# Optimization experiments

Hardware: AMD Instinct MI355X
Metric: run time of the kernel (lower is better)

Reference implementation:

```python
import jax, jax.numpy as jnp
import numpy as np
import math

D_MODEL, D_STATE, D_CONV = 1024, 16, 4
D_INNER = 2 * D_MODEL
DT_RANK = math.ceil(D_MODEL / 16)
B, L = 4, 2048


def setup_inputs() -> dict:
    key = jax.random.key(0)
    ks = jax.random.split(key, 10)
    s = 0.02
    x = jax.random.normal(ks[0], (B, L, D_MODEL), dtype=jnp.float32)
    ln_g = jnp.ones((D_MODEL,), jnp.float32)
    ln_b = jnp.zeros((D_MODEL,), jnp.float32)
    W_in = jax.random.normal(ks[1], (D_MODEL, 2 * D_INNER), jnp.float32) * s
    conv_w = jax.random.normal(ks[2], (D_INNER, 1, D_CONV), jnp.float32) * s
    conv_b = jnp.zeros((D_INNER,), jnp.float32)
    W_xp = jax.random.normal(ks[3], (D_INNER, DT_RANK + 2 * D_STATE), jnp.float32) * s
    W_dt = jax.random.normal(ks[4], (DT_RANK, D_INNER), jnp.float32) * (DT_RANK ** -0.5)
    # inverse-softplus of dt ~ 0.01 (between dt_min=0.001 and dt_max=0.1)
    dt_bias = jnp.full((D_INNER,), float(np.log(np.expm1(0.01))), jnp.float32)
    # S4D-real init: A = 1..d_state per channel
    A_log = jnp.log(jnp.broadcast_to(jnp.arange(1, D_STATE + 1, dtype=jnp.float32), (D_INNER, D_STATE)))
    D_skip = jnp.ones((D_INNER,), jnp.float32)
    W_out = jax.random.normal(ks[5], (D_INNER, D_MODEL), jnp.float32) * s
    return dict(x=x, ln_g=ln_g, ln_b=ln_b, W_in=W_in, conv_w=conv_w, conv_b=conv_b,
                W_xp=W_xp, W_dt=W_dt, dt_bias=dt_bias, A_log=A_log, D_skip=D_skip, W_out=W_out)


def _layernorm(x, g, b, eps=1e-5):
    m = jnp.mean(x, axis=-1, keepdims=True)
    v = jnp.mean(jnp.square(x - m), axis=-1, keepdims=True)
    return (x - m) * jax.lax.rsqrt(v + eps) * g + b


def _mamba(xn, W_in, conv_w, conv_b, W_xp, W_dt, dt_bias, A_log, D_skip, W_out):
    # xn: [B, L, d_model]
    xz = xn @ W_in                                   # [B, L, 2*d_inner]
    xi, z = jnp.split(xz, 2, axis=-1)                # each [B, L, d_inner]
    # depthwise causal conv over sequence
    xi_t = jnp.transpose(xi, (0, 2, 1))              # [B, d_inner, L]
    xc = jax.lax.conv_general_dilated(
        xi_t, conv_w, window_strides=(1,), padding=[(D_CONV - 1, 0)],
        feature_group_count=D_INNER, dimension_numbers=('NCH', 'OIH', 'NCH'))
    xc = jnp.transpose(xc, (0, 2, 1)) + conv_b       # [B, L, d_inner]
    xc = jax.nn.silu(xc)
    # input-dependent dt, B, C
    x_dbl = xc @ W_xp                                # [B, L, dt_rank + 2*d_state]
    dt_lo, Bm, Cm = jnp.split(x_dbl, [DT_RANK, DT_RANK + D_STATE], axis=-1)
    delta = jax.nn.softplus(dt_lo @ W_dt + dt_bias)  # [B, L, d_inner]
    A = -jnp.exp(A_log)                              # [d_inner, d_state]

    def step(h, inp):
        dt_t, B_t, C_t, u_t = inp                    # [B,D], [B,N], [B,N], [B,D]
        dA = jnp.exp(dt_t[..., None] * A)            # [B, D, N]
        h = h * dA + (dt_t * u_t)[..., None] * B_t[:, None, :]
        y = jnp.einsum('bdn,bn->bd', h, C_t)
        return h, y

    h0 = jnp.zeros((xn.shape[0], D_INNER, D_STATE), xn.dtype)
    inputs = (jnp.transpose(delta, (1, 0, 2)), jnp.transpose(Bm, (1, 0, 2)),
              jnp.transpose(Cm, (1, 0, 2)), jnp.transpose(xc, (1, 0, 2)))
    _, ys = jax.lax.scan(step, h0, inputs)           # ys: [L, B, d_inner]
    y = jnp.transpose(ys, (1, 0, 2)) + xc * D_skip   # [B, L, d_inner]
    y = y * jax.nn.silu(z)
    return y @ W_out                                 # [B, L, d_model]


def reference(x, ln_g, ln_b, W_in, conv_w, conv_b, W_xp, W_dt, dt_bias, A_log, D_skip, W_out):
    xn = _layernorm(x, ln_g, ln_b)
    return _mamba(xn, W_in, conv_w, conv_b, W_xp, W_dt, dt_bias, A_log, D_skip, W_out) + x
```

## Files before the change

### kernel.cpp

```cpp
#include <hip/hip_runtime.h>

#define DM 1024
#define DI 2048
#define DS 16
#define DTR 64
#define LL 2048
#define NROW 8192

typedef unsigned short u16;
typedef unsigned int u32;
typedef __bf16 bf16x8 __attribute__((ext_vector_type(8)));
typedef float f32x4 __attribute__((ext_vector_type(4)));
typedef float v2f __attribute__((ext_vector_type(2)));

__device__ __forceinline__ float bf2f(u16 u) {
  unsigned int v = ((unsigned int)u) << 16;
  return __builtin_bit_cast(float, v);
}
__device__ __forceinline__ u16 f2bf(float f) {
  unsigned int x = __builtin_bit_cast(unsigned int, f);
  x = x + 0x7fffu + ((x >> 16) & 1u);
  return (u16)(x >> 16);
}
__device__ __forceinline__ float lo_bf(u32 v) { return __builtin_bit_cast(float, v << 16); }
__device__ __forceinline__ float hi_bf(u32 v) { return __builtin_bit_cast(float, v & 0xFFFF0000u); }
__device__ __forceinline__ u32 pack_bf(float a, float b) {
  return (u32)f2bf(a) | ((u32)f2bf(b) << 16);
}
__device__ __forceinline__ bool io_f32(const u16* lng) { return lng[0] == 0; }

__device__ __forceinline__ void async16(const void* g, void* l) {
  __builtin_amdgcn_global_load_lds(
      (const __attribute__((address_space(1))) unsigned int*)g,
      (__attribute__((address_space(3))) unsigned int*)l, 16, 0, 0);
}

__device__ __forceinline__ void pow16v(float e1, v2f* E) {
  float e2 = e1 * e1;
  v2f sq = {e2, e2};
  E[0] = (v2f){e1, e2};
#pragma unroll
  for (int k = 1; k < 8; k++) E[k] = E[k - 1] * sq;
}

__device__ void transpose_dev(const void* __restrict__ in, u16* __restrict__ out,
                              int R, int C, int Cp, int bx, int by, bool f32,
                              int tid, u16 (*tile)[33]) {
  int c0 = bx * 32, r0 = by * 32;
  int tx = tid & 31, ty = tid >> 5;
#pragma unroll
  for (int i = 0; i < 4; i++) {
    int r = r0 + ty + i * 8, c = c0 + tx;
    u16 v = 0;
    if (r < R && c < C) {
      if (f32) v = f2bf(((const float*)in)[(size_t)r * C + c]);
      else     v = ((const u16*)in)[(size_t)r * C + c];
    }
    tile[ty + i * 8][tx] = v;
  }
  __syncthreads();
#pragma unroll
  for (int i = 0; i < 4; i++) {
    int oc = c0 + ty + i * 8, orr = r0 + tx;
    if (oc < Cp && orr < R) out[(size_t)oc * R + orr] = tile[tx][ty + i * 8];
  }
}

__global__ __launch_bounds__(256) void prep_k(
    const void* __restrict__ W_in, u16* __restrict__ W_inT,
    const void* __restrict__ W_dt, u16* __restrict__ W_dtT,
    const void* __restrict__ W_xp, u16* __restrict__ W_xpT,
    const void* __restrict__ W_out, u16* __restrict__ W_outT,
    const void* __restrict__ x, const u16* __restrict__ g,
    const u16* __restrict__ b, u16* __restrict__ xn) {
  __shared__ u16 tile[32][33];
  __shared__ float rs_[4], rq_[4];
  bool f32 = io_f32(g);
  int tid = threadIdx.x;
  int bid = blockIdx.x;
  if (bid < 4096) {
    transpose_dev(W_in, W_inT, 1024, 4096, 4096, bid & 127, bid >> 7, f32, tid, tile);
    return;
  } else if (bid < 4224) {
    bid -= 4096;
    transpose_dev(W_dt, W_dtT, 64, 2048, 2048, bid & 63, bid >> 6, f32, tid, tile);
    return;
  } else if (bid < 4480) {
    bid -= 4224;
    transpose_dev(W_xp, W_xpT, 2048, 96, 128, bid & 3, bid >> 2, f32, tid, tile);
    return;
  } else if (bid < 6528) {
    bid -= 4480;
    transpose_dev(W_out, W_outT, 2048, 1024, 1024, bid & 31, bid >> 5, f32, tid, tile);
    return;
  }
  int row = bid - 6528;
  float f[4];
  if (f32) {
    float4 v = ((const float4*)((const float*)x + (size_t)row * DM))[tid];
    f[0] = v.x; f[1] = v.y; f[2] = v.z; f[3] = v.w;
  } else {
    ushort4 v = ((const ushort4*)((const u16*)x + (size_t)row * DM))[tid];
    f[0] = bf2f(v.x); f[1] = bf2f(v.y); f[2] = bf2f(v.z); f[3] = bf2f(v.w);
  }
  float s = f[0] + f[1] + f[2] + f[3];
  float q = f[0] * f[0] + f[1] * f[1] + f[2] * f[2] + f[3] * f[3];
#pragma unroll
  for (int off = 32; off; off >>= 1) {
    s += __shfl_down(s, off, 64);
    q += __shfl_down(q, off, 64);
  }
  int wid = tid >> 6, lane = tid & 63;
  if (lane == 0) { rs_[wid] = s; rq_[wid] = q; }
  __syncthreads();
  float ts = rs_[0] + rs_[1] + rs_[2] + rs_[3];
  float tq = rq_[0] + rq_[1] + rq_[2] + rq_[3];
  float mean = ts * (1.f / DM);
  float var = tq * (1.f / DM) - mean * mean;
  float inv = rsqrtf(var + 1e-5f);
  int c = tid * 4;
  ushort4 o;
  u16* po = (u16*)&o;
#pragma unroll
  for (int k = 0; k < 4; k++) {
    float gk = f32 ? ((const float*)g)[c + k] : bf2f(g[c + k]);
    float bk = f32 ? ((const float*)b)[c + k] : bf2f(b[c + k]);
    po[k] = f2bf((f[k] - mean) * inv * gk + bk);
  }
  ((ushort4*)(xn + (size_t)row * DM))[tid] = o;
}

template <int EPI>
__device__ __forceinline__ void gemm_body(const u16* __restrict__ A,
                                          const u16* __restrict__ BT,
                                          void* __restrict__ C,
                                          const void* __restrict__ extra,
                                          int M, int N, int Klen, int ldk,
                                          const u16* __restrict__ lng, int mOff,
                                          u16* ldsA, u16* ldsB) {
  int tid = threadIdx.x;
  int wid = tid >> 6, lane = tid & 63;
  int l15 = lane & 15, quad = lane >> 4;
  int bm = blockIdx.x * 128;
  int bn;
  const u16* Ae = A;
  const u16* Be = BT;
  float* Cpart = nullptr;
  if (EPI == 5) {
    bn = 0;
    int ky = blockIdx.y;
    Ae += (size_t)ky * Klen;
    Be += (size_t)ky * Klen;
    Cpart = (float*)C + (size_t)ky * M * N;
  } else {
    bn = blockIdx.y * 128;
  }
  int wrow = (wid >> 1) * 64, wcol = (wid & 1) * 64;

  f32x4 zero = {0.f, 0.f, 0.f, 0.f};
  f32x4 acc[4][4];
#pragma unroll
  for (int i = 0; i < 4; i++)
#pragma unroll
    for (int j = 0; j < 4; j++) acc[i][j] = zero;

  int row0 = tid >> 2;
  int colb = (tid & 3) * 16;
  const char* Ap0 = (const char*)Ae + ((size_t)(bm + row0) * ldk) * 2 + colb;
  const char* Ap1 = (const char*)Ae + ((size_t)(bm + row0 + 64) * ldk) * 2 + colb;
  const char* Bp0 = (const char*)Be + ((size_t)(bn + row0) * ldk) * 2 + colb;
  const char* Bp1 = (const char*)Be + ((size_t)(bn + row0 + 64) * ldk) * 2 + colb;
  u16* la = ldsA + wid * 512;
  u16* lb = ldsB + wid * 512;

  for (int k0 = 0; k0 < Klen; k0 += 64) {
    size_t kb = (size_t)k0 * 2;
    async16(Ap0 + kb, la);
    async16(Ap1 + kb, la + 2048);
    async16(Ap0 + kb + 64, la + 4096);
    async16(Ap1 + kb + 64, la + 6144);
    async16(Bp0 + kb, lb);
    async16(Bp1 + kb, lb + 2048);
    async16(Bp0 + kb + 64, lb + 4096);
    async16(Bp1 + kb + 64, lb + 6144);
    __syncthreads();
#pragma unroll
    for (int s = 0; s < 2; s++) {
      bf16x8 af[4], bfr[4];
#pragma unroll
      for (int i = 0; i < 4; i++)
        af[i] = *(const bf16x8*)&ldsA[s * 4096 + (wrow + i * 16 + l15) * 32 + quad * 8];
#pragma unroll
      for (int j = 0; j < 4; j++)
        bfr[j] = *(const bf16x8*)&ldsB[s * 4096 + (wcol + j * 16 + l15) * 32 + quad * 8];
#pragma unroll
      for (int i = 0; i < 4; i++)
#pragma unroll
        for (int j = 0; j < 4; j++)
          acc[i][j] = __builtin_amdgcn_mfma_f32_16x16x32_bf16(af[i], bfr[j], acc[i][j], 0, 0, 0);
    }
    __syncthreads();
  }

  bool f32 = (EPI == 2 || EPI == 3) ? io_f32(lng) : false;
#pragma unroll
  for (int i = 0; i < 4; i++) {
#pragma unroll
    for (int j = 0; j < 4; j++) {
      int gn = bn + wcol + j * 16 + l15;
#pragma unroll
      for (int r = 0; r < 4; r++) {
        int gm = bm + wrow + i * 16 + quad * 4 + r;
        float v = acc[i][j][r];
        if (EPI == 2) {
          float bias = f32 ? ((const float*)extra)[gn] : bf2f(((const u16*)extra)[gn]);
          v += bias;
          float sp = (v > 20.f) ? v : log1pf(__expf(v));
          ((u16*)C)[(size_t)gm * N + gn] = f2bf(sp);
        } else if (EPI == 3) {
          size_t idx = (size_t)(gm + mOff) * N + gn;
          v += f32 ? ((const float*)extra)[idx] : bf2f(((const u16*)extra)[idx]);
          if (f32) ((float*)C)[idx] = v;
          else     ((u16*)C)[idx] = f2bf(v);
        } else {
          Cpart[(size_t)gm * N + gn] = v;
        }
      }
    }
  }
}

#define GEMM_WRAP(name, EPI)                                                        \
  __global__ __launch_bounds__(256) void name(                                      \
      const u16* __restrict__ A, const u16* __restrict__ BT, void* __restrict__ C,  \
      const void* __restrict__ extra, int M, int N, int Klen, int ldk,              \
      const u16* __restrict__ lng, int mOff) {                                      \
    __shared__ __align__(16) u16 ldsA[128 * 64];                                    \
    __shared__ __align__(16) u16 ldsB[128 * 64];                                    \
    gemm_body<EPI>(A, BT, C, extra, M, N, Klen, ldk, lng, mOff, ldsA, ldsB);        \
  }

GEMM_WRAP(gemm_xp_k, 5)
GEMM_WRAP(gemm_dt_k, 2)
GEMM_WRAP(gemm_out_k, 3)

__global__ __launch_bounds__(512, 2) void gemm_in256_k(
    const u16* __restrict__ A, const u16* __restrict__ BT,
    u16* __restrict__ C, u16* __restrict__ Z, int ldk, int Klen) {
  __shared__ __align__(16) u16 lds[65536];
  const int tid = threadIdx.x;
  const int wid = tid >> 6, lane = tid & 63;
  const int l15 = lane & 15, quad = lane >> 4;
  const int bm = blockIdx.x * 256, bn = blockIdx.y * 256;
  const int wrow = (wid >> 2) * 128;
  const int wcol = (wid & 3) * 64;

  const int srow = tid >> 3;
  const int sg = ((tid & 7) ^ (srow & 7)) * 8;
  const u16* Ag[4];
  const u16* Bg[4];
#pragma unroll
  for (int s = 0; s < 4; s++) {
    Ag[s] = A + (size_t)(bm + s * 64 + srow) * ldk + sg;
    Bg[s] = BT + (size_t)(bn + s * 64 + srow) * ldk + sg;
  }
  const int sdst = wid * 512;

  int rA[2], rB[2];
#pragma unroll
  for (int ks = 0; ks < 2; ks++) {
    int gsw = ((ks * 4 + quad) ^ (l15 & 7)) * 8;
    rA[ks] = (wrow + l15) * 64 + gsw;
    rB[ks] = 16384 + (wcol + l15) * 64 + gsw;
  }

  f32x4 acc[8][4];
  f32x4 zero = {0.f, 0.f, 0.f, 0.f};
#pragma unroll
  for (int i = 0; i < 8; i++)
#pragma unroll
    for (int j = 0; j < 4; j++) acc[i][j] = zero;

  const int NT = Klen >> 6;
  async16(Ag[0], &lds[sdst]);
  async16(Ag[1], &lds[4096 + sdst]);
  async16(Bg[0], &lds[16384 + sdst]);
  async16(Bg[1], &lds[16384 + 4096 + sdst]);
  async16(Bg[2], &lds[16384 + 8192 + sdst]);
  async16(Bg[3], &lds[16384 + 12288 + sdst]);
  async16(Ag[2], &lds[8192 + sdst]);
  async16(Ag[3], &lds[12288 + sdst]);
  if (NT > 1) {
    async16(Ag[0] + 64, &lds[32768 + sdst]);
    async16(Ag[1] + 64, &lds[32768 + 4096 + sdst]);
  }

  bf16x8 a[4][2], b0[2][2], b1[2][2];
  for (int t = 0; t < NT; ++t) {
    const int bb = (t & 1) << 15;
    const int nb = bb ^ 32768;
    const int k1 = (t + 1) << 6;
    const int k2 = (t + 2) << 6;
    const bool st1 = (t + 1 < NT), st2 = (t + 2 < NT);
    if (st1) asm volatile("s_waitcnt vmcnt(2)" ::: "memory");
    else     asm volatile("s_waitcnt vmcnt(0)" ::: "memory");
    __builtin_amdgcn_s_barrier();

#pragma unroll
    for (int mf = 0; mf < 4; mf++) {
      a[mf][0] = *(const bf16x8*)&lds[bb + rA[0] + mf * 1024];
      a[mf][1] = *(const bf16x8*)&lds[bb + rA[1] + mf * 1024];
    }
#pragma unroll
    for (int nf = 0; nf < 2; nf++) {
      b0[nf][0] = *(const bf16x8*)&lds[bb + rB[0] + nf * 1024];
      b0[nf][1] = *(const bf16x8*)&lds[bb + rB[1] + nf * 1024];
    }
    if (st1) {
      async16(Bg[0] + k1, &lds[nb + 16384 + sdst]);
      async16(Bg[1] + k1, &lds[nb + 16384 + 4096 + sdst]);
    }
    __builtin_amdgcn_s_barrier();
    asm volatile("s_waitcnt lgkmcnt(0)" ::: "memory");
    __builtin_amdgcn_s_setprio(1);
#pragma unroll
    for (int ks = 0; ks < 2; ks++)
#pragma unroll
      for (int mf = 0; mf < 4; mf++)
#pragma unroll
        for (int nf = 0; nf < 2; nf++)
          acc[mf][nf] = __builtin_amdgcn_mfma_f32_16x16x32_bf16(a[mf][ks], b0[nf][ks], acc[mf][nf], 0, 0, 0);
    __builtin_amdgcn_s_setprio(0);
    __builtin_amdgcn_s_barrier();

#pragma unroll
    for (int nf = 0; nf < 2; nf++) {
      b1[nf][0] = *(const bf16x8*)&lds[bb + rB[0] + (2 + nf) * 1024];
      b1[nf][1] = *(const bf16x8*)&lds[bb + rB[1] + (2 + nf) * 1024];
    }
    if (st1) {
      async16(Bg[2] + k1, &lds[nb + 16384 + 8192 + sdst]);
      async16(Bg[3] + k1, &lds[nb + 16384 + 12288 + sdst]);
    }
    __builtin_amdgcn_s_barrier();
    asm volatile("s_waitcnt lgkmcnt(0)" ::: "memory");
    __builtin_amdgcn_s_setprio(1);
#pragma unroll
    for (int ks = 0; ks < 2; ks++)
#pragma unroll
      for (int mf = 0; mf < 4; mf++)
#pragma unroll
        for (int nf = 0; nf < 2; nf++)
          acc[mf][2 + nf] = __builtin_amdgcn_mfma_f32_16x16x32_bf16(a[mf][ks], b1[nf][ks], acc[mf][2 + nf], 0, 0, 0);
    __builtin_amdgcn_s_setprio(0);
    __builtin_amdgcn_s_barrier();

#pragma unroll
    for (int mf = 0; mf < 4; mf++) {
      a[mf][0] = *(const bf16x8*)&lds[bb + rA[0] + 4096 + mf * 1024];
      a[mf][1] = *(const bf16x8*)&lds[bb + rA[1] + 4096 + mf * 1024];
    }
    if (st1) {
      async16(Ag[2] + k1, &lds[nb + 8192 + sdst]);
      async16(Ag[3] + k1, &lds[nb + 12288 + sdst]);
    }
    __builtin_amdgcn_s_barrier();
    asm volatile("s_waitcnt lgkmcnt(0)" ::: "memory");
    __builtin_amdgcn_s_setprio(1);
#pragma unroll
    for (int ks = 0; ks < 2; ks++)
#pragma unroll
      for (int mf = 0; mf < 4; mf++)
#pragma unroll
        for (int nf = 0; nf < 2; nf++)
          acc[4 + mf][2 + nf] = __builtin_amdgcn_mfma_f32_16x16x32_bf16(a[mf][ks], b1[nf][ks], acc[4 + mf][2 + nf], 0, 0, 0);
    __builtin_amdgcn_s_setprio(0);
    __builtin_amdgcn_s_barrier();

    if (st2) {
      async16(Ag[0] + k2, &lds[bb + sdst]);
      async16(Ag[1] + k2, &lds[bb + 4096 + sdst]);
    }
    __builtin_amdgcn_s_setprio(1);
#pragma unroll
    for (int ks = 0; ks < 2; ks++)
#pragma unroll
      for (int mf = 0; mf < 4; mf++)
#pragma unroll
        for (int nf = 0; nf < 2; nf++)
          acc[4 + mf][nf] = __builtin_amdgcn_mfma_f32_16x16x32_bf16(a[mf][ks], b0[nf][ks], acc[4 + mf][nf], 0, 0, 0);
    __builtin_amdgcn_s_setprio(0);
  }

#pragma unroll
  for (int i = 0; i < 8; i++) {
#pragma unroll
    for (int j = 0; j < 4; j++) {
      int gn = bn + wcol + j * 16 + l15;
#pragma unroll
      for (int r = 0; r < 4; r++) {
        int gm = bm + wrow + i * 16 + quad * 4 + r;
        float v = acc[i][j][r];
        if (gn < DI) {
          C[(size_t)gm * DI + gn] = f2bf(v);
        } else {
          float sv = v / (1.f + __expf(-v));
          Z[(size_t)gm * DI + (gn - DI)] = f2bf(sv);
        }
      }
    }
  }
}

__global__ __launch_bounds__(256) void conv4_k(const u16* __restrict__ xi,
                                               const void* __restrict__ cw,
                                               const void* __restrict__ cb,
                                               u16* __restrict__ xc,
                                               const u16* __restrict__ lng) {
  bool f32 = io_f32(lng);
  int idx = blockIdx.x * 256 + threadIdx.x;
  int c = idx & (DI - 1);
  int rq = idx >> 11;
  int l4 = (rq & (LL / 4 - 1)) * 4;
  int b = rq >> 9;
  float w[4], bias;
  if (f32) {
    float4 w4 = *(const float4*)((const float*)cw + (size_t)c * 4);
    w[0] = w4.x; w[1] = w4.y; w[2] = w4.z; w[3] = w4.w;
    bias = ((const float*)cb)[c];
  } else {
    ushort4 w4 = *(const ushort4*)((const u16*)cw + (size_t)c * 4);
    w[0] = bf2f(w4.x); w[1] = bf2f(w4.y); w[2] = bf2f(w4.z); w[3] = bf2f(w4.w);
    bias = bf2f(((const u16*)cb)[c]);
  }
  size_t base = ((size_t)(b * LL + l4)) * DI + c;
  float v[7];
#pragma unroll
  for (int j = 0; j < 7; j++) {
    int lj = l4 - 3 + j;
    v[j] = (lj >= 0) ? bf2f(xi[base + (size_t)(j - 3) * DI]) : 0.f;
  }
#pragma unroll
  for (int r = 0; r < 4; r++) {
    float acc = bias + v[r] * w[0] + v[r + 1] * w[1] + v[r + 2] * w[2] + v[r + 3] * w[3];
    float sv = acc / (1.f + __expf(-acc));
    xc[base + (size_t)r * DI] = f2bf(sv);
  }
}

__global__ __launch_bounds__(256) void reduce_dtlo_k(const float* __restrict__ Cpart,
                                                     float* __restrict__ xdbl,
                                                     u16* __restrict__ dtlo, int M) {
  int i = blockIdx.x * 256 + threadIdx.x;
  size_t MN = (size_t)M * 128;
  float v = Cpart[i] + Cpart[MN + i] + Cpart[2 * MN + i] + Cpart[3 * MN + i];
  xdbl[i] = v;
  int j = i & 127, m = i >> 7;
  if (j < 64) dtlo[(size_t)m * 64 + j] = f2bf(v);
}

__device__ __forceinline__ bool fastA(const void* A_log, bool f32, int d0) {
  bool fast = true;
#pragma unroll
  for (int c = 0; c < 2; c++)
    for (int n = 0; n < 16; n++) {
      float al = f32 ? ((const float*)A_log)[(d0 + c) * DS + n]
                     : bf2f(((const u16*)A_log)[(d0 + c) * DS + n]);
      float Av = __expf(al);
      fast = fast && (__builtin_fabsf(Av - (float)(n + 1)) <= 1e-3f * (n + 1));
    }
  return fast;
}

template <int S>
__global__ __launch_bounds__(256) void scan_p1(const u16* __restrict__ delta,
                                               const u16* __restrict__ xc,
                                               const float* __restrict__ xdbl,
                                               const void* __restrict__ A_log,
                                               const u16* __restrict__ lng,
                                               float* __restrict__ Pbuf,
                                               float* __restrict__ Lbuf,
                                               int NS) {
  bool f32 = io_f32(lng);
  int tid = threadIdx.x;
  int seg = blockIdx.x, dch = blockIdx.y, bL = blockIdx.z;
  int d0 = (dch * 256 + tid) * 2;
  size_t rb = (size_t)bL * LL;
  int l0 = seg * S;
  extern __shared__ float bc[];
#pragma unroll 2
  for (int i = tid; i < S * 4; i += 256) {
    int t = i >> 2, k = (i & 3) * 4;
    *(float4*)&bc[t * 16 + k] = *(const float4*)&xdbl[(rb + l0 + t) * 128 + 64 + k];
  }
  __syncthreads();
  size_t sb = ((((size_t)bL * NS + seg) * DI) + d0) * DS;
  const u32* dpu = (const u32*)(delta + (rb + l0) * DI + d0);
  const u32* upu = (const u32*)(xc + (rb + l0) * DI + d0);
  if (fastA(A_log, f32, d0)) {
    v2f h0[8], h1[8];
#pragma unroll
    for (int k = 0; k < 8; k++) { h0[k] = (v2f){0.f, 0.f}; h1[k] = (v2f){0.f, 0.f}; }
    float sum0 = 0.f, sum1 = 0.f;
    const int T = 8;
    for (int t0 = 0; t0 < S; t0 += T) {
      u32 dv[T], uv[T];
#pragma unroll
      for (int j = 0; j < T; j++) {
        dv[j] = dpu[j * (DI / 2)];
        uv[j] = upu[j * (DI / 2)];
      }
      dpu += T * (DI / 2);
      upu += T * (DI / 2);
#pragma unroll
      for (int j = 0; j < T; j++) {
        float dt0 = lo_bf(dv[j]), dt1 = hi_bf(dv[j]);
        float u0 = lo_bf(uv[j]), u1 = hi_bf(uv[j]);
        sum0 += dt0; sum1 += dt1;
        const v2f* B2 = (const v2f*)&bc[(t0 + j) * 16];
        v2f E[8];
        pow16v(__expf(-dt0), E);
        float com0 = dt0 * u0;
        v2f cv0 = {com0, com0};
#pragma unroll
        for (int k = 0; k < 8; k++) h0[k] = h0[k] * E[k] + B2[k] * cv0;
        pow16v(__expf(-dt1), E);
        float com1 = dt1 * u1;
        v2f cv1 = {com1, com1};
#pragma unroll
        for (int k = 0; k < 8; k++) h1[k] = h1[k] * E[k] + B2[k] * cv1;
      }
    }
    v2f P[8];
    pow16v(__expf(-sum0), P);
#pragma unroll
    for (int k = 0; k < 8; k++) { *(v2f*)&Pbuf[sb + 2 * k] = P[k]; *(v2f*)&Lbuf[sb + 2 * k] = h0[k]; }
    pow16v(__expf(-sum1), P);
#pragma unroll
    for (int k = 0; k < 8; k++) { *(v2f*)&Pbuf[sb + 16 + 2 * k] = P[k]; *(v2f*)&Lbuf[sb + 16 + 2 * k] = h1[k]; }
  } else {
    for (int c = 0; c < 2; c++) {
      int d = d0 + c;
      float A2[16], h[16], P[16];
#pragma unroll
      for (int n = 0; n < 16; n++) {
        float al = f32 ? ((const float*)A_log)[d * DS + n] : bf2f(((const u16*)A_log)[d * DS + n]);
        A2[n] = -__expf(al);
        h[n] = 0.f; P[n] = 1.f;
      }
      const u16* dp = delta + (rb + l0) * DI + d;
      const u16* up = xc + (rb + l0) * DI + d;
      for (int t = 0; t < S; t++) {
        float dt = bf2f(dp[(size_t)t * DI]);
        float u = bf2f(up[(size_t)t * DI]);
        float com = dt * u;
        const float* Bf = &bc[t * 16];
#pragma unroll
        for (int n = 0; n < 16; n++) {
          float dA = __expf(dt * A2[n]);
          h[n] = fmaf(h[n], dA, com * Bf[n]);
          P[n] *= dA;
        }
      }
#pragma unroll
      for (int n = 0; n < 16; n++) { Pbuf[sb + 16 * c + n] = P[n]; Lbuf[sb + 16 * c + n] = h[n]; }
    }
  }
}

__global__ __launch_bounds__(256) void scan_p2(float* __restrict__ Pbuf,
                                               float* __restrict__ Lbuf, int NS) {
  int idx = blockIdx.x * 256 + threadIdx.x;
  int bL = idx >> 15;
  int dn = idx & 32767;
  float H = 0.f;
  for (int s = 0; s < NS; s++) {
    size_t o = ((size_t)(bL * NS + s) << 15) + dn;
    float P = Pbuf[o], Lv = Lbuf[o];
    Lbuf[o] = H;
    H = fmaf(P, H, Lv);
  }
}

template <int S>
__global__ __launch_bounds__(256) void scan_p3(u16* __restrict__ dy,
                                               const u16* __restrict__ xc,
                                               const float* __restrict__ xdbl,
                                               const u16* __restrict__ z,
                                               const void* __restrict__ A_log,
                                               const void* __restrict__ D_skip,
                                               const u16* __restrict__ lng,
                                               const float* __restrict__ Lbuf,
                                               int NS) {
  bool f32 = io_f32(lng);
  int tid = threadIdx.x;
  int seg = blockIdx.x, dch = blockIdx.y, bL = blockIdx.z;
  int d0 = (dch * 256 + tid) * 2;
  size_t rb = (size_t)bL * LL;
  int l0 = seg * S;
  extern __shared__ float bc[];
#pragma unroll 2
  for (int i = tid; i < S * 8; i += 256) {
    int t = i >> 3, k = (i & 7) * 4;
    *(float4*)&bc[t * 32 + k] = *(const float4*)&xdbl[(rb + l0 + t) * 128 + 64 + k];
  }
  __syncthreads();
  size_t sb = ((((size_t)bL * NS + seg) * DI) + d0) * DS;
  float Dv0 = f32 ? ((const float*)D_skip)[d0] : bf2f(((const u16*)D_skip)[d0]);
  float Dv1 = f32 ? ((const float*)D_skip)[d0 + 1] : bf2f(((const u16*)D_skip)[d0 + 1]);
  u32* dpu = (u32*)(dy + (rb + l0) * DI + d0);
  const u32* upu = (const u32*)(xc + (rb + l0) * DI + d0);
  const u32* zpu = (const u32*)(z + (rb + l0) * DI + d0);
  if (fastA(A_log, f32, d0)) {
    v2f h0[8], h1[8];
#pragma unroll
    for (int k = 0; k < 8; k++) {
      h0[k] = *(const v2f*)&Lbuf[sb + 2 * k];
      h1[k] = *(const v2f*)&Lbuf[sb + 16 + 2 * k];
    }
    const int T = 8;
    for (int t0 = 0; t0 < S; t0 += T) {
      u32 dv[T], uv[T], zv[T];
#pragma unroll
      for (int j = 0; j < T; j++) {
        dv[j] = dpu[j * (DI / 2)];
        uv[j] = upu[j * (DI / 2)];
        zv[j] = zpu[j * (DI / 2)];
      }
      upu += T * (DI / 2);
      zpu += T * (DI / 2);
#pragma unroll
      for (int j = 0; j < T; j++) {
        float dt0 = lo_bf(dv[j]), dt1 = hi_bf(dv[j]);
        float u0 = lo_bf(uv[j]), u1 = hi_bf(uv[j]);
        float zg0 = lo_bf(zv[j]), zg1 = hi_bf(zv[j]);
        const v2f* B2 = (const v2f*)&bc[(t0 + j) * 32];
        const v2f* C2 = (const v2f*)&bc[(t0 + j) * 32 + 16];
        v2f E[8];
        pow16v(__expf(-dt0), E);
        float com0 = dt0 * u0;
        v2f cv = {com0, com0};
        v2f a0 = {0.f, 0.f}, a1 = {0.f, 0.f};
#pragma unroll
        for (int k = 0; k < 8; k += 2) {
          h0[k] = h0[k] * E[k] + B2[k] * cv;
          h0[k + 1] = h0[k + 1] * E[k + 1] + B2[k + 1] * cv;
          a0 += h0[k] * C2[k];
          a1 += h0[k + 1] * C2[k + 1];
        }
        float cs0 = (a0.x + a0.y) + (a1.x + a1.y);
        pow16v(__expf(-dt1), E);
        float com1 = dt1 * u1;
        cv = (v2f){com1, com1};
        a0 = (v2f){0.f, 0.f}; a1 = (v2f){0.f, 0.f};
#pragma unroll
        for (int k = 0; k < 8; k += 2) {
          h1[k] = h1[k] * E[k] + B2[k] * cv;
          h1[k + 1] = h1[k + 1] * E[k + 1] + B2[k + 1] * cv;
          a0 += h1[k] * C2[k];
          a1 += h1[k + 1] * C2[k + 1];
        }
        float cs1 = (a0.x + a0.y) + (a1.x + a1.y);
        float y0 = (cs0 + u0 * Dv0) * zg0;
        float y1 = (cs1 + u1 * Dv1) * zg1;
        dpu[j * (DI / 2)] = pack_bf(y0, y1);
      }
      dpu += T * (DI / 2);
    }
  } else {
    for (int c = 0; c < 2; c++) {
      int d = d0 + c;
      float A2[16], h[16];
#pragma unroll
      for (int n = 0; n < 16; n++) {
        float al = f32 ? ((const float*)A_log)[d * DS + n] : bf2f(((const u16*)A_log)[d * DS + n]);
        A2[n] = -__expf(al);
        h[n] = Lbuf[sb + 16 * c + n];
      }
      float Dv = (c == 0) ? Dv0 : Dv1;
      u16* dp = dy + (rb + l0) * DI + d;
      const u16* up = xc + (rb + l0) * DI + d;
      const u16* zp = z + (rb + l0) * DI + d;
      for (int t = 0; t < S; t++) {
        float dt = bf2f(dp[(size_t)t * DI]);
        float u = bf2f(up[(size_t)t * DI]);
        float zg = bf2f(zp[(size_t)t * DI]);
        float com = dt * u;
        const float* Bf = &bc[t * 32];
        const float* Cf = &bc[t * 32 + 16];
        float cs = 0.f;
#pragma unroll
        for (int n = 0; n < 16; n++) {
          float dA = __expf(dt * A2[n]);
          h[n] = fmaf(h[n], dA, com * Bf[n]);
          cs = fmaf(h[n], Cf[n], cs);
        }
        dp[(size_t)t * DI] = f2bf((cs + u * Dv) * zg);
      }
    }
  }
}

static void launch_scan(int NS, int nb, u16* xi, u16* xc, float* xdbl, u16* z,
                        const u16* A_log, const u16* D_sk, const u16* ln_g,
                        float* Pbuf, float* Lbuf, hipStream_t stream) {
  int S = LL / NS;
  dim3 g1(NS, 4, nb);
  if (S == 32) {
    scan_p1<32><<<g1, 256, 32 * 64, stream>>>(xi, xc, xdbl, A_log, ln_g, Pbuf, Lbuf, NS);
  } else if (S == 64) {
    scan_p1<64><<<g1, 256, 64 * 64, stream>>>(xi, xc, xdbl, A_log, ln_g, Pbuf, Lbuf, NS);
  } else {
    scan_p1<128><<<g1, 256, 128 * 64, stream>>>(xi, xc, xdbl, A_log, ln_g, Pbuf, Lbuf, NS);
  }
  scan_p2<<<nb * 128, 256, 0, stream>>>(Pbuf, Lbuf, NS);
  if (S == 32) {
    scan_p3<32><<<g1, 256, 32 * 128, stream>>>(xi, xc, xdbl, z, A_log, D_sk, ln_g, Lbuf, NS);
  } else if (S == 64) {
    scan_p3<64><<<g1, 256, 64 * 128, stream>>>(xi, xc, xdbl, z, A_log, D_sk, ln_g, Lbuf, NS);
  } else {
    scan_p3<128><<<g1, 256, 128 * 128, stream>>>(xi, xc, xdbl, z, A_log, D_sk, ln_g, Lbuf, NS);
  }
}

extern "C" void kernel_launch(void* const* d_in, const int* in_sizes, int n_in,
                              void* d_out, int out_size, void* d_ws, size_t ws_size,
                              hipStream_t stream) {
  const u16* x = (const u16*)d_in[0];
  const u16* ln_g = (const u16*)d_in[1];
  const u16* ln_b = (const u16*)d_in[2];
  const u16* W_in = (const u16*)d_in[3];
  const u16* cw = (const u16*)d_in[4];
  const u16* cb = (const u16*)d_in[5];
  const u16* W_xp = (const u16*)d_in[6];
  const u16* W_dt = (const u16*)d_in[7];
  const u16* dt_b = (const u16*)d_in[8];
  const u16* A_log = (const u16*)d_in[9];
  const u16* D_sk = (const u16*)d_in[10];
  const u16* W_out = (const u16*)d_in[11];

  char* ws = (char*)d_ws;
  const size_t MB = 1024 * 1024;

  if (ws_size >= 124 * MB) {
    int NS = (ws_size >= 180 * MB) ? 64 : (ws_size >= 144 * MB) ? 32 : 16;
    u16* xc = (u16*)(ws + 0);
    u16* xn = xc;
    u16* W_inT = (u16*)(ws + 16 * MB);
    u16* xi = (u16*)(ws + 32 * MB);
    u16* z = (u16*)(ws + 64 * MB);
    float* xdbl = (float*)(ws + 96 * MB);
    u16* dtlo = (u16*)(ws + 100 * MB);
    u16* W_xpT = (u16*)(ws + 101 * MB);
    u16* W_dtT = (u16*)(ws + 102 * MB);
    u16* W_outT = (u16*)(ws + 103 * MB);
    size_t stateSz = (size_t)NS * 4 * DI * DS * 4;
    float* Cpart = (float*)(ws + 107 * MB);
    float* Pbuf = (float*)(ws + 107 * MB);
    float* Lbuf = (float*)(ws + 107 * MB + stateSz);

    prep_k<<<6528 + NROW, 256, 0, stream>>>(W_in, W_inT, W_dt, W_dtT, W_xp, W_xpT,
                                            W_out, W_outT, x, ln_g, ln_b, xn);
    gemm_in256_k<<<dim3(NROW / 256, (2 * DI) / 256), 512, 0, stream>>>(xn, W_inT, xi, z, DM, DM);
    conv4_k<<<(NROW / 4 * DI) / 256, 256, 0, stream>>>(xi, cw, cb, xc, ln_g);
    gemm_xp_k<<<dim3(64, 4), 256, 0, stream>>>(xc, W_xpT, Cpart, nullptr, NROW, 128, 512, DI, ln_g, 0);
    reduce_dtlo_k<<<(NROW * 128) / 256, 256, 0, stream>>>(Cpart, xdbl, dtlo, NROW);
    gemm_dt_k<<<dim3(64, 16), 256, 0, stream>>>(dtlo, W_dtT, xi, dt_b, NROW, DI, DTR, DTR, ln_g, 0);
    launch_scan(NS, 4, xi, xc, xdbl, z, A_log, D_sk, ln_g, Pbuf, Lbuf, stream);
    gemm_out_k<<<dim3(64, 8), 256, 0, stream>>>(xi, W_outT, d_out, x, NROW, DM, DI, DI, ln_g, 0);
  } else {
    int NS = 32;
    u16* W_inT = (u16*)(ws + 0);
    u16* W_xpT = (u16*)(ws + 8 * MB);
    u16* W_dtT = (u16*)(ws + 9 * MB);
    u16* W_outT = (u16*)(ws + 10 * MB);
    u16* xn = (u16*)(ws + 14 * MB);
    u16* xi = (u16*)(ws + 30 * MB);
    u16* z = (u16*)(ws + 38 * MB);
    u16* xc = (u16*)(ws + 46 * MB);
    float* xdbl = (float*)(ws + 54 * MB);
    u16* dtlo = (u16*)(ws + 55 * MB);
    float* Cpart = (float*)(ws + 56 * MB);
    float* Pbuf = (float*)(ws + 56 * MB);
    float* Lbuf = (float*)(ws + 61 * MB);

    prep_k<<<6528 + NROW, 256, 0, stream>>>(W_in, W_inT, W_dt, W_dtT, W_xp, W_xpT,
                                            W_out, W_outT, x, ln_g, ln_b, xn);
    for (int b = 0; b < 4; b++) {
      const u16* xnb = xn + (size_t)b * LL * DM;
      gemm_in256_k<<<dim3(LL / 256, (2 * DI) / 256), 512, 0, stream>>>(xnb, W_inT, xi, z, DM, DM);
      conv4_k<<<(LL / 4 * DI) / 256, 256, 0, stream>>>(xi, cw, cb, xc, ln_g);
      gemm_xp_k<<<dim3(16, 4), 256, 0, stream>>>(xc, W_xpT, Cpart, nullptr, LL, 128, 512, DI, ln_g, 0);
      reduce_dtlo_k<<<(LL * 128) / 256, 256, 0, stream>>>(Cpart, xdbl, dtlo, LL);
      gemm_dt_k<<<dim3(16, 16), 256, 0, stream>>>(dtlo, W_dtT, xi, dt_b, LL, DI, DTR, DTR, ln_g, 0);
      launch_scan(NS, 1, xi, xc, xdbl, z, A_log, D_sk, ln_g, Pbuf, Lbuf, stream);
      gemm_out_k<<<dim3(16, 8), 256, 0, stream>>>(xi, W_outT, d_out, x, LL, DM, DI, DI, ln_g, b * LL);
    }
  }
}
```

Measured before the change: 523.6 us.

## Restructure GEMM main loop with register-prefetched fragments and one barrier per tile

Rewrites the in-projection GEMM K-loop so each tile is loaded as a whole stage, A and B together, two stages ahead. LDS fragments for the next tile are read into registers while MFMAs for the current tile are still running. The four barriers per iteration become one barrier plus a full vmcnt(0) wait. This aims to cut barrier stalls and hide LDS read latency, at the cost of more live registers (aLo/aHi split) and a coarser global-load wait that may expose memory latency.

```diff
diff --git a/kernel.cpp b/kernel.cpp
--- a/kernel.cpp
+++ b/kernel.cpp
@@ -284,102 +284,92 @@
   const int NT = Klen >> 6;
   async16(Ag[0], &lds[sdst]);
   async16(Ag[1], &lds[4096 + sdst]);
-  async16(Bg[0], &lds[16384 + sdst]);
-  async16(Bg[1], &lds[16384 + 4096 + sdst]);
-  async16(Bg[2], &lds[16384 + 8192 + sdst]);
-  async16(Bg[3], &lds[16384 + 12288 + sdst]);
   async16(Ag[2], &lds[8192 + sdst]);
   async16(Ag[3], &lds[12288 + sdst]);
+  async16(Bg[0], &lds[16384 + sdst]);
+  async16(Bg[1], &lds[20480 + sdst]);
+  async16(Bg[2], &lds[24576 + sdst]);
+  async16(Bg[3], &lds[28672 + sdst]);
   if (NT > 1) {
     async16(Ag[0] + 64, &lds[32768 + sdst]);
-    async16(Ag[1] + 64, &lds[32768 + 4096 + sdst]);
-  }
-
-  bf16x8 a[4][2], b0[2][2], b1[2][2];
+    async16(Ag[1] + 64, &lds[36864 + sdst]);
+    async16(Ag[2] + 64, &lds[40960 + sdst]);
+    async16(Ag[3] + 64, &lds[45056 + sdst]);
+    async16(Bg[0] + 64, &lds[49152 + sdst]);
+    async16(Bg[1] + 64, &lds[53248 + sdst]);
+    async16(Bg[2] + 64, &lds[57344 + sdst]);
+    async16(Bg[3] + 64, &lds[61440 + sdst]);
+  }
+  asm volatile("s_waitcnt vmcnt(8)" ::: "memory");
+  __builtin_amdgcn_s_barrier();
+  __builtin_amdgcn_sched_barrier(0);
+
+  bf16x8 aLo[4][2], aHi[4][2], b0[2][2], b1[2][2];
+#pragma unroll
+  for (int mf = 0; mf < 4; mf++) {
+    aLo[mf][0] = *(const bf16x8*)&lds[rA[0] + mf * 1024];
+    aLo[mf][1] = *(const bf16x8*)&lds[rA[1] + mf * 1024];
+  }
+#pragma unroll
+  for (int nf = 0; nf < 2; nf++)
+#pragma unroll
+    for (int ks = 0; ks < 2; ks++) {
+      b0[nf][ks] = *(const bf16x8*)&lds[rB[ks] + nf * 1024];
+      b1[nf][ks] = *(const bf16x8*)&lds[rB[ks] + (2 + nf) * 1024];
+    }
+
   for (int t = 0; t < NT; ++t) {
     const int bb = (t & 1) << 15;
     const int nb = bb ^ 32768;
-    const int k1 = (t + 1) << 6;
     const int k2 = (t + 2) << 6;
     const bool st1 = (t + 1 < NT), st2 = (t + 2 < NT);
-    if (st1) asm volatile("s_waitcnt vmcnt(2)" ::: "memory");
-    else     asm volatile("s_waitcnt vmcnt(0)" ::: "memory");
+
+    __builtin_amdgcn_s_setprio(1);
+#pragma unroll
+    for (int ks = 0; ks < 2; ks++)
+#pragma unroll
+      for (int mf = 0; mf < 4; mf++)
+#pragma unroll
+        for (int nf = 0; nf < 2; nf++)
+          acc[mf][nf] = __builtin_amdgcn_mfma_f32_16x16x32_bf16(aLo[mf][ks], b0[nf][ks], acc[mf][nf], 0, 0, 0);
+    __builtin_amdgcn_s_setprio(0);
+#pragma unroll
+    for (int mf = 0; mf < 4; mf++) {
+      aHi[mf][0] = *(const bf16x8*)&lds[bb + rA[0] + 4096 + mf * 1024];
+      aHi[mf][1] = *(const bf16x8*)&lds[bb + rA[1] + 4096 + mf * 1024];
+    }
+    __builtin_amdgcn_s_setprio(1);
+#pragma unroll
+    for (int ks = 0; ks < 2; ks++)
+#pragma unroll
+      for (int mf = 0; mf < 4; mf++)
+#pragma unroll
+        for (int nf = 0; nf < 2; nf++)
+          acc[mf][2 + nf] = __builtin_amdgcn_mfma_f32_16x16x32_bf16(aLo[mf][ks], b1[nf][ks], acc[mf][2 + nf], 0, 0, 0);
+    __builtin_amdgcn_s_setprio(0);
+
+    asm volatile("s_waitcnt lgkmcnt(0)" ::: "memory");
+    __builtin_amdgcn_sched_barrier(0);
+    asm volatile("s_waitcnt vmcnt(0)" ::: "memory");
     __builtin_amdgcn_s_barrier();
-
-#pragma unroll
-    for (int mf = 0; mf < 4; mf++) {
-      a[mf][0] = *(const bf16x8*)&lds[bb + rA[0] + mf * 1024];
-      a[mf][1] = *(const bf16x8*)&lds[bb + rA[1] + mf * 1024];
-    }
-#pragma unroll
-    for (int nf = 0; nf < 2; nf++) {
-      b0[nf][0] = *(const bf16x8*)&lds[bb + rB[0] + nf * 1024];
-      b0[nf][1] = *(const bf16x8*)&lds[bb + rB[1] + nf * 1024];
-    }
-    if (st1) {
-      async16(Bg[0] + k1, &lds[nb + 16384 + sdst]);
-      async16(Bg[1] + k1, &lds[nb + 16384 + 4096 + sdst]);
-    }
-    __builtin_amdgcn_s_barrier();
-    asm volatile("s_waitcnt lgkmcnt(0)" ::: "memory");
-    __builtin_amdgcn_s_setprio(1);
-#pragma unroll
-    for (int ks = 0; ks < 2; ks++)
-#pragma unroll
-      for (int mf = 0; mf < 4; mf++)
-#pragma unroll
-        for (int nf = 0; nf < 2; nf++)
-          acc[mf][nf] = __builtin_amdgcn_mfma_f32_16x16x32_bf16(a[mf][ks], b0[nf][ks], acc[mf][nf], 0, 0, 0);
-    __builtin_amdgcn_s_setprio(0);
-    __builtin_amdgcn_s_barrier();
-
-#pragma unroll
-    for (int nf = 0; nf < 2; nf++) {
-      b1[nf][0] = *(const bf16x8*)&lds[bb + rB[0] + (2 + nf) * 1024];
-      b1[nf][1] = *(const bf16x8*)&lds[bb + rB[1] + (2 + nf) * 1024];
-    }
-    if (st1) {
-      async16(Bg[2] + k1, &lds[nb + 16384 + 8192 + sdst]);
-      async16(Bg[3] + k1, &lds[nb + 16384 + 12288 + sdst]);
-    }
-    __builtin_amdgcn_s_barrier();
-    asm volatile("s_waitcnt lgkmcnt(0)" ::: "memory");
-    __builtin_amdgcn_s_setprio(1);
-#pragma unroll
-    for (int ks = 0; ks < 2; ks++)
-#pragma unroll
-      for (int mf = 0; mf < 4; mf++)
-#pragma unroll
-        for (int nf = 0; nf < 2; nf++)
-          acc[mf][2 + nf] = __builtin_amdgcn_mfma_f32_16x16x32_bf16(a[mf][ks], b1[nf][ks], acc[mf][2 + nf], 0, 0, 0);
-    __builtin_amdgcn_s_setprio(0);
-    __builtin_amdgcn_s_barrier();
-
-#pragma unroll
-    for (int mf = 0; mf < 4; mf++) {
-      a[mf][0] = *(const bf16x8*)&lds[bb + rA[0] + 4096 + mf * 1024];
-      a[mf][1] = *(const bf16x8*)&lds[bb + rA[1] + 4096 + mf * 1024];
-    }
-    if (st1) {
-      async16(Ag[2] + k1, &lds[nb + 8192 + sdst]);
-      async16(Ag[3] + k1, &lds[nb + 12288 + sdst]);
-    }
-    __builtin_amdgcn_s_barrier();
-    asm volatile("s_waitcnt lgkmcnt(0)" ::: "memory");
-    __builtin_amdgcn_s_setprio(1);
-#pragma unroll
-    for (int ks = 0; ks < 2; ks++)
-#pragma unroll
-      for (int mf = 0; mf < 4; mf++)
-#pragma unroll
-        for (int nf = 0; nf < 2; nf++)
-          acc[4 + mf][2 + nf] = __builtin_amdgcn_mfma_f32_16x16x32_bf16(a[mf][ks], b1[nf][ks], acc[4 + mf][2 + nf], 0, 0, 0);
-    __builtin_amdgcn_s_setprio(0);
-    __builtin_amdgcn_s_barrier();
+    __builtin_amdgcn_sched_barrier(0);
 
     if (st2) {
       async16(Ag[0] + k2, &lds[bb + sdst]);
       async16(Ag[1] + k2, &lds[bb + 4096 + sdst]);
+      async16(Ag[2] + k2, &lds[bb + 8192 + sdst]);
+      async16(Ag[3] + k2, &lds[bb + 12288 + sdst]);
+      async16(Bg[0] + k2, &lds[bb + 16384 + sdst]);
+      async16(Bg[1] + k2, &lds[bb + 20480 + sdst]);
+      async16(Bg[2] + k2, &lds[bb + 24576 + sdst]);
+      async16(Bg[3] + k2, &lds[bb + 28672 + sdst]);
+    }
+    if (st1) {
+#pragma unroll
+      for (int mf = 0; mf < 4; mf++) {
+        aLo[mf][0] = *(const bf16x8*)&lds[nb + rA[0] + mf * 1024];
+        aLo[mf][1] = *(const bf16x8*)&lds[nb + rA[1] + mf * 1024];
+      }
     }
     __builtin_amdgcn_s_setprio(1);
 #pragma unroll
@@ -388,8 +378,31 @@
       for (int mf = 0; mf < 4; mf++)
 #pragma unroll
         for (int nf = 0; nf < 2; nf++)
-          acc[4 + mf][nf] = __builtin_amdgcn_mfma_f32_16x16x32_bf16(a[mf][ks], b0[nf][ks], acc[4 + mf][nf], 0, 0, 0);
+          acc[4 + mf][nf] = __builtin_amdgcn_mfma_f32_16x16x32_bf16(aHi[mf][ks], b0[nf][ks], acc[4 + mf][nf], 0, 0, 0);
     __builtin_amdgcn_s_setprio(0);
+    if (st1) {
+#pragma unroll
+      for (int nf = 0; nf < 2; nf++)
+#pragma unroll
+        for (int ks = 0; ks < 2; ks++)
+          b0[nf][ks] = *(const bf16x8*)&lds[nb + rB[ks] + nf * 1024];
+    }
+    __builtin_amdgcn_s_setprio(1);
+#pragma unroll
+    for (int ks = 0; ks < 2; ks++)
+#pragma unroll
+      for (int mf = 0; mf < 4; mf++)
+#pragma unroll
+        for (int nf = 0; nf < 2; nf++)
+          acc[4 + mf][2 + nf] = __builtin_amdgcn_mfma_f32_16x16x32_bf16(aHi[mf][ks], b1[nf][ks], acc[4 + mf][2 + nf], 0, 0, 0);
+    __builtin_amdgcn_s_setprio(0);
+    if (st1) {
+#pragma unroll
+      for (int nf = 0; nf < 2; nf++)
+#pragma unroll
+        for (int ks = 0; ks < 2; ks++)
+          b1[nf][ks] = *(const bf16x8*)&lds[nb + rB[ks] + (2 + nf) * 1024];
+    }
   }
 
 #pragma unroll
```

Result: no change. 524.9 us (+0.2%).
